# Kernel tuning notes

Hardware: AMD Instinct MI355X
Metric: run time of the kernel (lower is better)

The kernel has to match this reference:

```python
import jax, jax.numpy as jnp
import numpy as np


def _hfft3(x):
    # sequential Hermitian FFT along the 3 spatial axes; each axis n -> 2*(n-1)
    for ax in (2, 3, 4):
        x = jnp.fft.hfft(x, axis=ax)
    return x


def _ihfft3(x):
    # sequential inverse Hermitian FFT; ihfft requires real input, so take real
    # part before each application (mirrors numpy semantics on the original code)
    for ax in (2, 3, 4):
        x = jnp.fft.ihfft(jnp.real(x), axis=ax)
    return x


def setup_inputs() -> dict:
    key = jax.random.key(0)
    k1, k2 = jax.random.split(key)
    B, Cin, Cout = 4, 32, 32
    D1 = D2 = D3 = 64
    m1 = m2 = m3 = 16
    scale = 1.0 / (Cin * Cout)
    x = jax.random.normal(k1, (B, Cin, D1, D2, D3), dtype=jnp.float32)
    weights1 = scale * jax.random.uniform(k2, (Cin, Cout, m1, m2, m3), dtype=jnp.float32)
    return {"x": x, "weights1": weights1}


def reference(x, weights1):
    B = x.shape[0]
    D1, D2, D3 = x.shape[2], x.shape[3], x.shape[4]
    Cout = weights1.shape[1]
    m1, m2, m3 = weights1.shape[2], weights1.shape[3], weights1.shape[4]

    # 3D Hartley-style transform: [B,Cin,2(D1-1),2(D2-1),2(D3-1)] real
    x_ht = _hfft3(x)

    # mode truncation + channel mixing on low modes only
    low = jnp.einsum("bixyz,ioxyz->boxyz", x_ht[:, :, :m1, :m2, :m3], weights1)

    out_ht = jnp.zeros((B, Cout, D1, D2, D3 // 2 + 1), dtype=x.dtype)
    out_ht = out_ht.at[:, :, :m1, :m2, :m3].set(low)

    # inverse transform -> complex [B,Cout,D1//2+1,D2//2+1,(D3//2+1)//2+1]
    out = _ihfft3(out_ht)
    # return real/imag stacked so output is real-valued
    return jnp.stack([out.real, out.imag], axis=-1)
```

## Files before the change

kernel.cpp:

```cpp
#include <hip/hip_runtime.h>
#include <hip/hip_bf16.h>


#define PI2 6.283185307179586476925f

__global__ void k_init(float* __restrict__ Tmat, float* __restrict__ cA,
                       float* __restrict__ cB, float* __restrict__ sB) {
    int t = blockIdx.x * 256 + threadIdx.x;
    if (t < 1024) {
        int k = t >> 6, j = t & 63;
        float w = (j == 0 || j == 63) ? 1.f : 2.f;
        int r = (j * k) % 126;
        Tmat[t] = w * cosf(PI2 * (float)r / 126.f);
    }
    if (t < 528) {
        int p = t >> 4, j = t & 15;
        int r = (j * p) % 64;
        cA[t] = cosf(PI2 * (float)r / 64.f) * (1.f / 64.f);
    }
    if (t < 272) {
        int p = t >> 4, j = t & 15;
        int r = (j * p) % 33;
        float a = PI2 * (float)r / 33.f;
        cB[t] = cosf(a) * (1.f / 33.f);
        sB[t] = sinf(a) * (1.f / 33.f);
    }
}

__global__ __launch_bounds__(256) void k_fwd12(const float* __restrict__ x,
                                               const float* __restrict__ Tmat,
                                               float* __restrict__ A2) {
    __shared__ float xt[64 * 68];
    __shared__ float Ts[16 * 68];
    __shared__ float tmp[16 * 68];
    const int j1 = blockIdx.x, bc = blockIdx.y;
    const int t = threadIdx.x;

    float4* xt4 = (float4*)xt;
    float4* Ts4 = (float4*)Ts;
    const float4* xg = (const float4*)(x + ((size_t)bc * 64 + j1) * 4096);
    for (int c = t; c < 1024; c += 256) {
        int j2 = c >> 4, q = c & 15;
        xt4[j2 * 17 + q] = xg[c];
    }
    if (t < 256) {
        const float4* Tg = (const float4*)Tmat;
        int k = t >> 4, q = t & 15;
        Ts4[k * 17 + q] = Tg[t];
    }
    __syncthreads();

    {
        const int j2 = (t & 15) + 16 * (t >> 6);
        const int k3b = (t >> 4) & 3;
        float acc[4] = {0.f, 0.f, 0.f, 0.f};
#pragma unroll 4
        for (int q = 0; q < 16; q++) {
            float4 xv = xt4[j2 * 17 + q];
#pragma unroll
            for (int c = 0; c < 4; c++) {
                float4 tv = Ts4[(k3b + 4 * c) * 17 + q];
                acc[c] += xv.x * tv.x + xv.y * tv.y + xv.z * tv.z + xv.w * tv.w;
            }
        }
#pragma unroll
        for (int c = 0; c < 4; c++)
            tmp[(k3b + 4 * c) * 68 + j2] = acc[c];
    }
    __syncthreads();

    {
        const int k3 = t & 15;
        const int k2 = t >> 4;
        const float4* tmp4 = (const float4*)tmp;
        float acc = 0.f;
#pragma unroll 4
        for (int q = 0; q < 16; q++) {
            float4 tv = tmp4[k3 * 17 + q];
            float4 Tv = Ts4[k2 * 17 + q];
            acc += tv.x * Tv.x + tv.y * Tv.y + tv.z * Tv.z + tv.w * Tv.w;
        }
        A2[((size_t)bc * 64 + j1) * 256 + t] = acc;
    }
}

__global__ __launch_bounds__(256) void k_fwd3(const float* __restrict__ A2,
                                              const float* __restrict__ Tmat,
                                              float* __restrict__ X) {
    __shared__ float Ts[128];
    const int k1g = blockIdx.x;
    const int bc = blockIdx.y;
    const int t = threadIdx.x;
    if (t < 128) Ts[t] = Tmat[k1g * 128 + t];
    __syncthreads();
    const float* Ap = A2 + (size_t)bc * 64 * 256 + t;
    float a0 = 0.f, a1 = 0.f;
#pragma unroll 8
    for (int j1 = 0; j1 < 64; j1++) {
        float v = Ap[j1 * 256];
        a0 += v * Ts[j1];
        a1 += v * Ts[64 + j1];
    }
    X[(size_t)bc * 4096 + (size_t)(k1g * 2) * 256 + t] = a0;
    X[(size_t)bc * 4096 + (size_t)(k1g * 2 + 1) * 256 + t] = a1;
}

__global__ __launch_bounds__(256) void k_mix(const float* __restrict__ X,
                                             const float* __restrict__ W,
                                             float* __restrict__ low) {
    const int mc = blockIdx.x;
    const int o = blockIdx.y;
    const int m = mc * 256 + threadIdx.x;
    const float* Xp = X + m;
    const float* Wp = W + (size_t)o * 4096 + m;
    float acc[4] = {0.f, 0.f, 0.f, 0.f};
#pragma unroll 4
    for (int i = 0; i < 32; i++) {
        float wv = Wp[(size_t)i * 32 * 4096];
#pragma unroll
        for (int b = 0; b < 4; b++)
            acc[b] += Xp[(size_t)(b * 32 + i) * 4096] * wv;
    }
#pragma unroll
    for (int b = 0; b < 4; b++)
        low[((size_t)(b * 32 + o)) * 4096 + m] = acc[b];
}

__global__ __launch_bounds__(256) void k_inv(const float* __restrict__ low,
                                             const float* __restrict__ cA,
                                             const float* __restrict__ cB,
                                             const float* __restrict__ sB,
                                             float* __restrict__ out) {
    __shared__ float lt[4096];
    __shared__ float c1[256];
    __shared__ float c2[528];
    __shared__ float cAs[528], cBs[272], sBs[272];
    const int p1 = blockIdx.x, bo = blockIdx.y;
    const int t = threadIdx.x;

    float4* lt4 = (float4*)lt;
    const float4* lg = (const float4*)(low + (size_t)bo * 4096);
    for (int c = t; c < 1024; c += 256) lt4[c] = lg[c];
    for (int c = t; c < 528; c += 256) cAs[c] = cA[c];
    for (int c = t; c < 272; c += 256) { cBs[c] = cB[c]; sBs[c] = sB[c]; }
    __syncthreads();

    {
        float acc = 0.f;
#pragma unroll
        for (int k1 = 0; k1 < 16; k1++) acc += lt[(k1 << 8) + t] * cAs[p1 * 16 + k1];
        c1[t] = acc;
    }
    __syncthreads();

    for (int idx = t; idx < 528; idx += 256) {
        int p2 = idx >> 4, k3 = idx & 15;
        float acc = 0.f;
#pragma unroll
        for (int k2 = 0; k2 < 16; k2++) acc += c1[(k2 << 4) + k3] * cAs[p2 * 16 + k2];
        c2[idx] = acc;
    }
    __syncthreads();

    float* op = out + ((size_t)bo * 33 + p1) * 33 * 17 * 2;
    for (int idx = t; idx < 1122; idx += 256) {
        int p2 = idx / 34, rem = idx % 34;
        int p3 = rem >> 1, cc = rem & 1;
        const float* M = cc ? sBs : cBs;
        float acc = 0.f;
#pragma unroll
        for (int k3 = 0; k3 < 16; k3++) acc += c2[(p2 << 4) + k3] * M[p3 * 16 + k3];
        op[idx] = acc;
    }
}

extern "C" void kernel_launch(void* const* d_in, const int* in_sizes, int n_in,
                              void* d_out, int out_size, void* d_ws, size_t ws_size,
                              hipStream_t stream) {
    const float* x = (const float*)d_in[0];
    const float* W = (const float*)d_in[1];
    float* out = (float*)d_out;

    float* ws = (float*)d_ws;
    float* Tmat = ws;
    float* cA   = ws + 1024;
    float* cB   = ws + 1552;
    float* sB   = ws + 1824;
    float* A2   = ws + 4096;
    float* X    = A2 + 2097152;
    float* low  = X + 524288;

    k_init<<<dim3(4), dim3(256), 0, stream>>>(Tmat, cA, cB, sB);
    k_fwd12<<<dim3(64, 128), dim3(256), 0, stream>>>(x, Tmat, A2);
    k_fwd3<<<dim3(8, 128), dim3(256), 0, stream>>>(A2, Tmat, X);
    k_mix<<<dim3(16, 32), dim3(256), 0, stream>>>(X, W, low);
    k_inv<<<dim3(33, 128), dim3(256), 0, stream>>>(low, cA, cB, sB, out);
}
```

Measured before the change: 249.1 us.

## Split inverse transform into three kernels and use wave-uniform transposed T in fwd12

The fused per-(p1,bo) inverse kernel, which reloaded the whole 4096-element low block for each of 33 p1 values, is replaced by three staged kernels (E, F, G). Each keeps its inputs in registers and loops over output modes, writing intermediates to global workspace. In k_fwd12 the first-stage contraction now reads a transposed coefficient table with a wave-uniform index, so each wave computes four output rows from broadcast loads. This trades redundant loads and LDS traffic for extra launches and intermediate global round-trips.

```diff
diff --git a/kernel.cpp b/kernel.cpp
--- a/kernel.cpp
+++ b/kernel.cpp
@@ -1,17 +1,19 @@
 #include <hip/hip_runtime.h>
-#include <hip/hip_bf16.h>
 
 
 #define PI2 6.283185307179586476925f
 
-__global__ void k_init(float* __restrict__ Tmat, float* __restrict__ cA,
-                       float* __restrict__ cB, float* __restrict__ sB) {
+__global__ void k_init(float* __restrict__ Tmat, float* __restrict__ Tt,
+                       float* __restrict__ cA, float* __restrict__ cB,
+                       float* __restrict__ sB) {
     int t = blockIdx.x * 256 + threadIdx.x;
     if (t < 1024) {
         int k = t >> 6, j = t & 63;
         float w = (j == 0 || j == 63) ? 1.f : 2.f;
         int r = (j * k) % 126;
-        Tmat[t] = w * cosf(PI2 * (float)r / 126.f);
+        float v = w * cosf(PI2 * (float)r / 126.f);
+        Tmat[t] = v;
+        Tt[j * 16 + k] = v;
     }
     if (t < 528) {
         int p = t >> 4, j = t & 15;
@@ -29,6 +31,7 @@
 
 __global__ __launch_bounds__(256) void k_fwd12(const float* __restrict__ x,
                                                const float* __restrict__ Tmat,
+                                               const float* __restrict__ Tt,
                                                float* __restrict__ A2) {
     __shared__ float xt[64 * 68];
     __shared__ float Ts[16 * 68];
@@ -43,7 +46,7 @@
         int j2 = c >> 4, q = c & 15;
         xt4[j2 * 17 + q] = xg[c];
     }
-    if (t < 256) {
+    {
         const float4* Tg = (const float4*)Tmat;
         int k = t >> 4, q = t & 15;
         Ts4[k * 17 + q] = Tg[t];
@@ -51,21 +54,26 @@
     __syncthreads();
 
     {
-        const int j2 = (t & 15) + 16 * (t >> 6);
-        const int k3b = (t >> 4) & 3;
-        float acc[4] = {0.f, 0.f, 0.f, 0.f};
+        const int j2 = t & 63;
+        const int w = __builtin_amdgcn_readfirstlane(t >> 6);
+        const float4* Tt4 = (const float4*)Tt;
+        float a0 = 0.f, a1 = 0.f, a2 = 0.f, a3 = 0.f;
 #pragma unroll 4
         for (int q = 0; q < 16; q++) {
             float4 xv = xt4[j2 * 17 + q];
-#pragma unroll
-            for (int c = 0; c < 4; c++) {
-                float4 tv = Ts4[(k3b + 4 * c) * 17 + q];
-                acc[c] += xv.x * tv.x + xv.y * tv.y + xv.z * tv.z + xv.w * tv.w;
-            }
+            float4 t0 = Tt4[(4 * q + 0) * 4 + w];
+            float4 t1 = Tt4[(4 * q + 1) * 4 + w];
+            float4 t2 = Tt4[(4 * q + 2) * 4 + w];
+            float4 t3 = Tt4[(4 * q + 3) * 4 + w];
+            a0 += xv.x * t0.x + xv.y * t1.x + xv.z * t2.x + xv.w * t3.x;
+            a1 += xv.x * t0.y + xv.y * t1.y + xv.z * t2.y + xv.w * t3.y;
+            a2 += xv.x * t0.z + xv.y * t1.z + xv.z * t2.z + xv.w * t3.z;
+            a3 += xv.x * t0.w + xv.y * t1.w + xv.z * t2.w + xv.w * t3.w;
         }
-#pragma unroll
-        for (int c = 0; c < 4; c++)
-            tmp[(k3b + 4 * c) * 68 + j2] = acc[c];
+        tmp[(4 * w + 0) * 68 + j2] = a0;
+        tmp[(4 * w + 1) * 68 + j2] = a1;
+        tmp[(4 * w + 2) * 68 + j2] = a2;
+        tmp[(4 * w + 3) * 68 + j2] = a3;
     }
     __syncthreads();
 
@@ -126,51 +134,73 @@
         low[((size_t)(b * 32 + o)) * 4096 + m] = acc[b];
 }
 
-__global__ __launch_bounds__(256) void k_inv(const float* __restrict__ low,
-                                             const float* __restrict__ cA,
-                                             const float* __restrict__ cB,
-                                             const float* __restrict__ sB,
-                                             float* __restrict__ out) {
-    __shared__ float lt[4096];
-    __shared__ float c1[256];
-    __shared__ float c2[528];
-    __shared__ float cAs[528], cBs[272], sBs[272];
-    const int p1 = blockIdx.x, bo = blockIdx.y;
+__global__ __launch_bounds__(256) void k_invE(const float* __restrict__ low,
+                                              const float* __restrict__ cA,
+                                              float* __restrict__ E) {
+    const int bo = blockIdx.y;
     const int t = threadIdx.x;
-
-    float4* lt4 = (float4*)lt;
-    const float4* lg = (const float4*)(low + (size_t)bo * 4096);
-    for (int c = t; c < 1024; c += 256) lt4[c] = lg[c];
-    for (int c = t; c < 528; c += 256) cAs[c] = cA[c];
-    for (int c = t; c < 272; c += 256) { cBs[c] = cB[c]; sBs[c] = sB[c]; }
-    __syncthreads();
-
-    {
+    const float* lp = low + (size_t)bo * 4096 + t;
+    float r[16];
+#pragma unroll
+    for (int k1 = 0; k1 < 16; k1++) r[k1] = lp[k1 * 256];
+    const int p1q = blockIdx.x;
+    const int p1lo = p1q * 8 + (p1q > 0 ? 1 : 0);
+    const int p1hi = p1q * 8 + 8;
+    for (int p1 = p1lo; p1 <= p1hi; p1++) {
         float acc = 0.f;
 #pragma unroll
-        for (int k1 = 0; k1 < 16; k1++) acc += lt[(k1 << 8) + t] * cAs[p1 * 16 + k1];
-        c1[t] = acc;
-    }
-    __syncthreads();
-
-    for (int idx = t; idx < 528; idx += 256) {
-        int p2 = idx >> 4, k3 = idx & 15;
+        for (int k1 = 0; k1 < 16; k1++) acc += r[k1] * cA[p1 * 16 + k1];
+        E[((size_t)bo * 33 + p1) * 256 + t] = acc;
+    }
+}
+
+__global__ __launch_bounds__(256) void k_invF(const float* __restrict__ E,
+                                              const float* __restrict__ cA,
+                                              float* __restrict__ F) {
+    const int gid = blockIdx.x * 256 + threadIdx.x;
+    const int bo = gid / 528;
+    const int rem = gid - bo * 528;
+    const int p1 = rem >> 4;
+    const int k3 = rem & 15;
+    const float* ep = E + ((size_t)bo * 33 + p1) * 256 + k3;
+    float r[16];
+#pragma unroll
+    for (int k2 = 0; k2 < 16; k2++) r[k2] = ep[k2 * 16];
+    const int h = blockIdx.y;
+    const int p2lo = h * 17;
+    const int p2hi = h ? 32 : 16;
+    float* fp = F + (((size_t)bo * 33 + p1) * 33) * 16 + k3;
+    for (int p2 = p2lo; p2 <= p2hi; p2++) {
         float acc = 0.f;
 #pragma unroll
-        for (int k2 = 0; k2 < 16; k2++) acc += c1[(k2 << 4) + k3] * cAs[p2 * 16 + k2];
-        c2[idx] = acc;
-    }
-    __syncthreads();
-
-    float* op = out + ((size_t)bo * 33 + p1) * 33 * 17 * 2;
-    for (int idx = t; idx < 1122; idx += 256) {
-        int p2 = idx / 34, rem = idx % 34;
-        int p3 = rem >> 1, cc = rem & 1;
-        const float* M = cc ? sBs : cBs;
-        float acc = 0.f;
-#pragma unroll
-        for (int k3 = 0; k3 < 16; k3++) acc += c2[(p2 << 4) + k3] * M[p3 * 16 + k3];
-        op[idx] = acc;
+        for (int k2 = 0; k2 < 16; k2++) acc += r[k2] * cA[p2 * 16 + k2];
+        fp[(size_t)p2 * 16] = acc;
+    }
+}
+
+__global__ __launch_bounds__(256) void k_invG(const float* __restrict__ F,
+                                              const float* __restrict__ cB,
+                                              const float* __restrict__ sB,
+                                              float* __restrict__ out) {
+    const int gid = blockIdx.x * 256 + threadIdx.x;
+    if (gid >= 128 * 33 * 33) return;
+    const float4* rf4 = (const float4*)(F + (size_t)gid * 16);
+    float rf[16];
+    float4 f;
+    f = rf4[0]; rf[0] = f.x; rf[1] = f.y; rf[2] = f.z; rf[3] = f.w;
+    f = rf4[1]; rf[4] = f.x; rf[5] = f.y; rf[6] = f.z; rf[7] = f.w;
+    f = rf4[2]; rf[8] = f.x; rf[9] = f.y; rf[10] = f.z; rf[11] = f.w;
+    f = rf4[3]; rf[12] = f.x; rf[13] = f.y; rf[14] = f.z; rf[15] = f.w;
+    float* op = out + (size_t)gid * 34;
+    for (int p3 = 0; p3 < 17; p3++) {
+        float ac = 0.f, as = 0.f;
+#pragma unroll
+        for (int k3 = 0; k3 < 16; k3++) {
+            ac += rf[k3] * cB[p3 * 16 + k3];
+            as += rf[k3] * sB[p3 * 16 + k3];
+        }
+        op[p3 * 2] = ac;
+        op[p3 * 2 + 1] = as;
     }
 }
 
@@ -183,16 +213,21 @@
 
     float* ws = (float*)d_ws;
     float* Tmat = ws;
-    float* cA   = ws + 1024;
-    float* cB   = ws + 1552;
-    float* sB   = ws + 1824;
+    float* Tt   = ws + 1024;
+    float* cA   = ws + 2048;
+    float* cB   = ws + 2576;
+    float* sB   = ws + 2848;
     float* A2   = ws + 4096;
     float* X    = A2 + 2097152;
     float* low  = X + 524288;
-
-    k_init<<<dim3(4), dim3(256), 0, stream>>>(Tmat, cA, cB, sB);
-    k_fwd12<<<dim3(64, 128), dim3(256), 0, stream>>>(x, Tmat, A2);
+    float* E    = low + 524288;
+    float* F    = E + 1081344;
+
+    k_init<<<dim3(4), dim3(256), 0, stream>>>(Tmat, Tt, cA, cB, sB);
+    k_fwd12<<<dim3(64, 128), dim3(256), 0, stream>>>(x, Tmat, Tt, A2);
     k_fwd3<<<dim3(8, 128), dim3(256), 0, stream>>>(A2, Tmat, X);
     k_mix<<<dim3(16, 32), dim3(256), 0, stream>>>(X, W, low);
-    k_inv<<<dim3(33, 128), dim3(256), 0, stream>>>(low, cA, cB, sB, out);
-}
+    k_invE<<<dim3(4, 128), dim3(256), 0, stream>>>(low, cA, E);
+    k_invF<<<dim3(264, 2), dim3(256), 0, stream>>>(E, cA, F);
+    k_invG<<<dim3(545), dim3(256), 0, stream>>>(F, cB, sB, out);
+}
```

After: 269.8 us. 8.3% more time.
